# Kernel optimization log

Hardware: AMD Instinct MI355X
Metric: run time of the kernel (lower is better)

## Reference

```python
import jax, jax.numpy as jnp
import numpy as np

A, D, F = 2048, 64, 12  # atoms, depth, filter_length


def _chemconv(x, conn, bond, filters):
    # x: (A, D); conn: (A, A, F); bond: (A, F, 2); filters: (D, F, D+2)
    # node_connection = conn.transpose(1,2) @ x -> (A, F, D)
    ncon = jnp.einsum('anf,nd->afd', conn, x)
    combined = jnp.concatenate([ncon, bond], axis=2)  # (A, F, D+2)
    # broadcast-multiply by filters then sum over last two dims -> (A, out_depth)
    return jnp.einsum('afc,ofc->ao', combined, filters)


def setup_inputs() -> dict:
    key = jax.random.key(0)
    k1, k2, k3, k4, k5 = jax.random.split(key, 5)
    x = jax.random.normal(k1, (A, D), dtype=jnp.float32)
    conn = jax.random.uniform(k2, (A, A, F), dtype=jnp.float32)
    bond = jax.random.normal(k3, (A, F, 2), dtype=jnp.float32)
    scale = 1.0 / D  # filters.data.normal_() * (1/in_depth)
    f0 = jax.random.normal(k4, (D, F, D + 2), dtype=jnp.float32) * scale
    f1 = jax.random.normal(k5, (D, F, D + 2), dtype=jnp.float32) * scale
    return {
        'node_property_tensor': x,
        'connectivity_tensor': conn,
        'bond_property_tensor': bond,
        'filters0': f0,
        'filters1': f1,
    }


def reference(node_property_tensor, connectivity_tensor, bond_property_tensor, filters0, filters1):
    x = node_property_tensor
    out = x
    for filt in (filters0, filters1):
        # each ChemConv layer is applied twice (same weights), per the torch code
        out = jax.nn.relu(_chemconv(out, connectivity_tensor, bond_property_tensor, filt))
        out = _chemconv(out, connectivity_tensor, bond_property_tensor, filt)
        out = out + x  # residual to the original block input
        out = jax.nn.relu(out)
    return out
```

## Files before the change

### kernel.cpp

```cpp
#include <hip/hip_runtime.h>


#define A_N 2048
#define D_N 64
#define F_N 12
#define K_TOTAL (A_N * F_N)
#define NSPLIT 48
#define KSEG (K_TOTAL / NSPLIT)
#define BK 64
#define NKB (KSEG / BK)

typedef short short8 __attribute__((ext_vector_type(8)));
typedef float f32x16 __attribute__((ext_vector_type(16)));

#define GLOAD16(ldsp, gp)                                                        \
  __builtin_amdgcn_global_load_lds(                                              \
      (const __attribute__((address_space(1))) void*)(gp),                       \
      (__attribute__((address_space(3))) void*)(ldsp), 16, 0, 0)

__device__ __forceinline__ unsigned pk_bf16(float a, float b) {
  unsigned ua = __float_as_uint(a);
  unsigned ub = __float_as_uint(b);
  ua += 0x7fffu + ((ua >> 16) & 1u);
  ub += 0x7fffu + ((ub >> 16) & 1u);
  return (ua >> 16) | (ub & 0xffff0000u);
}

__global__ void k_conv(const float* __restrict__ conn, uint4* __restrict__ connb) {
  size_t i = (size_t)blockIdx.x * 256 + threadIdx.x;
  const float4* src = (const float4*)conn + i * 2;
  float4 c0 = src[0];
  float4 c1 = src[1];
  uint4 o;
  o.x = pk_bf16(c0.x, c0.y);
  o.y = pk_bf16(c0.z, c0.w);
  o.z = pk_bf16(c1.x, c1.y);
  o.w = pk_bf16(c1.z, c1.w);
  connb[i] = o;
}

__global__ void k_transpose_x(const float* __restrict__ x, float* __restrict__ xt) {
  __shared__ float ld[64][65];
  int m0 = blockIdx.x * 64;
  int t = threadIdx.x;
  int r = t >> 2, cq = (t & 3) * 16;
  const float4* src = (const float4*)(x + (size_t)(m0 + r) * 64 + cq);
#pragma unroll
  for (int i = 0; i < 4; ++i) {
    float4 v = src[i];
    ld[r][cq + i * 4 + 0] = v.x;
    ld[r][cq + i * 4 + 1] = v.y;
    ld[r][cq + i * 4 + 2] = v.z;
    ld[r][cq + i * 4 + 3] = v.w;
  }
  __syncthreads();
  int c = t >> 2, ml0 = (t & 3) * 16;
  float4* dst = (float4*)(xt + (size_t)c * 2048 + m0 + ml0);
#pragma unroll
  for (int i = 0; i < 4; ++i) {
    float4 v;
    v.x = ld[ml0 + i * 4 + 0][c];
    v.y = ld[ml0 + i * 4 + 1][c];
    v.z = ld[ml0 + i * 4 + 2][c];
    v.w = ld[ml0 + i * 4 + 3][c];
    dst[i] = v;
  }
}

__global__ void k_bterm(const float* __restrict__ bond, const float* __restrict__ f0,
                        const float* __restrict__ f1, float* __restrict__ bt0,
                        float* __restrict__ bt1) {
  int a = blockIdx.x * 64 + (threadIdx.x & 63);
  int o = blockIdx.y * 4 + (threadIdx.x >> 6);
  float s0 = 0.f, s1 = 0.f;
#pragma unroll
  for (int f = 0; f < F_N; ++f) {
#pragma unroll
    for (int j = 0; j < 2; ++j) {
      float bv = bond[a * 24 + f * 2 + j];
      s0 += bv * f0[o * 792 + f * 66 + 64 + j];
      s1 += bv * f1[o * 792 + f * 66 + 64 + j];
    }
  }
  bt0[o * 2048 + a] = s0;
  bt1[o * 2048 + a] = s1;
}

__global__ void k_g(const float* __restrict__ vt, const float* __restrict__ filt,
                    unsigned* __restrict__ gt ) {
  __shared__ float W[12][64];
  int o = blockIdx.y;
  int t = threadIdx.x;
  for (int i = t; i < 768; i += 256) W[i >> 6][i & 63] = filt[o * 792 + (i >> 6) * 66 + (i & 63)];
  __syncthreads();
  int n = blockIdx.x * 256 + t;
  float acc[12] = {0.f, 0.f, 0.f, 0.f, 0.f, 0.f, 0.f, 0.f, 0.f, 0.f, 0.f, 0.f};
#pragma unroll 4
  for (int d = 0; d < 64; ++d) {
    float v = vt[d * 2048 + n];
#pragma unroll
    for (int f = 0; f < F_N; ++f) acc[f] += v * W[f][d];
  }
  unsigned* dst = gt + ((size_t)o * K_TOTAL + n * 12) / 2;
#pragma unroll
  for (int i = 0; i < 6; ++i) dst[i] = pk_bf16(acc[2 * i], acc[2 * i + 1]);
}

__launch_bounds__(256, 3)
__global__ void k_big(const unsigned short* __restrict__ connb,
                      const unsigned short* __restrict__ gt, float* __restrict__ part) {
  __shared__ __align__(16) unsigned short smem[24576];
  int t = threadIdx.x, lane = t & 63, w = t >> 6;
  int m0 = blockIdx.x * 128;
  int k0 = blockIdx.y * KSEG;

  int rl = lane >> 3;
  int cs = (lane & 7) ^ rl;

  const unsigned short* cG[4];
  unsigned short* cL[4];
#pragma unroll
  for (int j = 0; j < 4; ++j) {
    int r = w * 32 + j * 8 + rl;
    cG[j] = connb + (size_t)(m0 + r) * K_TOTAL + k0 + cs * 8;
    cL[j] = smem + (w * 32 + j * 8) * 64;
  }
  const unsigned short* gG[2];
  unsigned short* gL[2];
#pragma unroll
  for (int j = 0; j < 2; ++j) {
    int r = w * 16 + j * 8 + rl;
    gG[j] = gt + (size_t)r * K_TOTAL + k0 + cs * 8;
    gL[j] = smem + 16384 + (w * 16 + j * 8) * 64;
  }

  f32x16 acc0, acc1;
#pragma unroll
  for (int i = 0; i < 16; ++i) { acc0[i] = 0.f; acc1[i] = 0.f; }

  int oh = w >> 1, ah = w & 1;
  int orow = oh * 32 + (lane & 31);
  int arow = ah * 64 + (lane & 31);
  int sw = lane & 7;
  int khalf = lane >> 5;

#pragma unroll
  for (int j = 0; j < 4; ++j) GLOAD16(cL[j], cG[j]);
#pragma unroll
  for (int j = 0; j < 2; ++j) GLOAD16(gL[j], gG[j]);

  for (int kb = 0; kb < NKB; ++kb) {
    __syncthreads();
    if (kb + 1 < NKB) {
      int ko = (kb + 1) * 64;
      int b = (kb + 1) & 1;
#pragma unroll
      for (int j = 0; j < 4; ++j) GLOAD16(cL[j] + b * 8192, cG[j] + ko);
#pragma unroll
      for (int j = 0; j < 2; ++j) GLOAD16(gL[j] + b * 4096, gG[j] + ko);
    }
    const unsigned short* cb = smem + (kb & 1) * 8192;
    const unsigned short* gb = smem + 16384 + (kb & 1) * 4096;
#pragma unroll
    for (int kk = 0; kk < 4; ++kk) {
      int c = kk * 2 + khalf;
      int coff = ((c ^ sw) << 3);
      short8 af = *(const short8*)(gb + orow * 64 + coff);
      short8 b0 = *(const short8*)(cb + arow * 64 + coff);
      short8 b1 = *(const short8*)(cb + (arow + 32) * 64 + coff);
      acc0 = __builtin_amdgcn_mfma_f32_32x32x16_bf16(af, b0, acc0, 0, 0, 0);
      acc1 = __builtin_amdgcn_mfma_f32_32x32x16_bf16(af, b1, acc1, 0, 0, 0);
    }
  }

  float* pp = part + (size_t)blockIdx.y * (64 * 2048);
  int a0 = m0 + ah * 64 + (lane & 31);
  int ob = oh * 32 + 4 * khalf;
#pragma unroll
  for (int rg = 0; rg < 16; ++rg) {
    int o = ob + (rg & 3) + 8 * (rg >> 2);
    pp[o * 2048 + a0] = acc0[rg];
    pp[o * 2048 + a0 + 32] = acc1[rg];
  }
}

__global__ void k_reduce(const float* __restrict__ part, const float* __restrict__ bt,
                         const float* __restrict__ xt, float* __restrict__ curt,
                         float* __restrict__ outp, int residual, int final_layer) {
  int idx = blockIdx.x * 256 + threadIdx.x;
  float s = bt[idx];
#pragma unroll
  for (int sI = 0; sI < NSPLIT; ++sI) s += part[(size_t)sI * (64 * 2048) + idx];
  if (residual) s += xt[idx];
  s = fmaxf(s, 0.f);
  curt[idx] = s;
  if (final_layer) {
    int o = idx >> 11, m = idx & 2047;
    outp[m * 64 + o] = s;
  }
}

extern "C" void kernel_launch(void* const* d_in, const int* in_sizes, int n_in,
                              void* d_out, int out_size, void* d_ws, size_t ws_size,
                              hipStream_t stream) {
  const float* x    = (const float*)d_in[0];
  const float* conn = (const float*)d_in[1];
  const float* bond = (const float*)d_in[2];
  const float* f0   = (const float*)d_in[3];
  const float* f1   = (const float*)d_in[4];
  float* out = (float*)d_out;

  char* ws = (char*)d_ws;
  float* xt   = (float*)(ws + 0);
  float* curt = (float*)(ws + 524288);
  float* bt0  = (float*)(ws + 1048576);
  float* bt1  = (float*)(ws + 1572864);
  unsigned short* gt = (unsigned short*)(ws + 2097152);
  float* part = (float*)(ws + 5242880);
  unsigned short* connb = (unsigned short*)(ws + 33554432);

  k_conv<<<24576, 256, 0, stream>>>(conn, (uint4*)connb);
  k_transpose_x<<<32, 256, 0, stream>>>(x, xt);
  k_bterm<<<dim3(32, 16), 256, 0, stream>>>(bond, f0, f1, bt0, bt1);

  for (int layer = 0; layer < 4; ++layer) {
    const float* filt = (layer < 2) ? f0 : f1;
    const float* bt   = (layer < 2) ? bt0 : bt1;
    const float* vin  = (layer == 0) ? xt : curt;
    k_g<<<dim3(8, 64), 256, 0, stream>>>(vin, filt, (unsigned*)gt);
    k_big<<<dim3(16, NSPLIT), 256, 0, stream>>>(connb, gt, part);
    k_reduce<<<512, 256, 0, stream>>>(part, bt, xt, curt, out, layer & 1, layer == 3);
  }
}
```

Before: 493.6 us.

## Pre-tile bf16 connectivity and g operands into contiguous per-block K-segment layout

```diff
diff --git a/kernel.cpp b/kernel.cpp
--- a/kernel.cpp
+++ b/kernel.cpp
@@ -26,17 +26,31 @@
   return (ua >> 16) | (ub & 0xffff0000u);
 }
 
-__global__ void k_conv(const float* __restrict__ conn, uint4* __restrict__ connb) {
-  size_t i = (size_t)blockIdx.x * 256 + threadIdx.x;
-  const float4* src = (const float4*)conn + i * 2;
-  float4 c0 = src[0];
-  float4 c1 = src[1];
-  uint4 o;
-  o.x = pk_bf16(c0.x, c0.y);
-  o.y = pk_bf16(c0.z, c0.w);
-  o.z = pk_bf16(c1.x, c1.y);
-  o.w = pk_bf16(c1.z, c1.w);
-  connb[i] = o;
+__device__ __forceinline__ unsigned short bf16_1(float v) {
+  unsigned u = __float_as_uint(v);
+  u += 0x7fffu + ((u >> 16) & 1u);
+  return (unsigned short)(u >> 16);
+}
+
+__global__ void k_conv(const float* __restrict__ conn, unsigned short* __restrict__ connt) {
+  int atile = blockIdx.x, ks = blockIdx.y;
+  int t = threadIdx.x, lane = t & 63, w = t >> 6;
+  unsigned short* tile = connt + (size_t)(atile * 48 + ks) * 65536;
+  int kb = lane >> 3, j = lane & 7;
+#pragma unroll 4
+  for (int p = 0; p < 32; ++p) {
+    int row = w * 32 + p;
+    const float4* src = (const float4*)(conn + (size_t)(atile * 128 + row) * K_TOTAL +
+                                        ks * 512 + lane * 8);
+    float4 a = src[0];
+    float4 b = src[1];
+    uint4 o;
+    o.x = pk_bf16(a.x, a.y);
+    o.y = pk_bf16(a.z, a.w);
+    o.z = pk_bf16(b.x, b.y);
+    o.w = pk_bf16(b.z, b.w);
+    *(uint4*)(tile + ((kb * 128 + row) * 8 + j) * 8) = o;
+  }
 }
 
 __global__ void k_transpose_x(const float* __restrict__ x, float* __restrict__ xt) {
@@ -87,7 +101,7 @@
 }
 
 __global__ void k_g(const float* __restrict__ vt, const float* __restrict__ filt,
-                    unsigned* __restrict__ gt ) {
+                    unsigned short* __restrict__ gtt) {
   __shared__ float W[12][64];
   int o = blockIdx.y;
   int t = threadIdx.x;
@@ -101,37 +115,38 @@
 #pragma unroll
     for (int f = 0; f < F_N; ++f) acc[f] += v * W[f][d];
   }
-  unsigned* dst = gt + ((size_t)o * K_TOTAL + n * 12) / 2;
-#pragma unroll
-  for (int i = 0; i < 6; ++i) dst[i] = pk_bf16(acc[2 * i], acc[2 * i + 1]);
+  int kbase = n * 12;
+#pragma unroll
+  for (int f = 0; f < F_N; ++f) {
+    int k = kbase + f;
+    int ks = k >> 9, kb = (k >> 6) & 7, c = k & 63;
+    gtt[(((size_t)ks * 8 + kb) * 64 + o) * 64 + c] = bf16_1(acc[f]);
+  }
 }
 
 __launch_bounds__(256, 3)
-__global__ void k_big(const unsigned short* __restrict__ connb,
-                      const unsigned short* __restrict__ gt, float* __restrict__ part) {
+__global__ void k_big(const unsigned short* __restrict__ connt,
+                      const unsigned short* __restrict__ gtt, float* __restrict__ part) {
   __shared__ __align__(16) unsigned short smem[24576];
   int t = threadIdx.x, lane = t & 63, w = t >> 6;
-  int m0 = blockIdx.x * 128;
-  int k0 = blockIdx.y * KSEG;
-
-  int rl = lane >> 3;
-  int cs = (lane & 7) ^ rl;
-
-  const unsigned short* cG[4];
-  unsigned short* cL[4];
+  int atile = blockIdx.x, ks = blockIdx.y;
+  const unsigned short* ct = connt + (size_t)(atile * 48 + ks) * 65536;
+  const unsigned short* gs = gtt + (size_t)ks * 32768;
+
+  int rl = lane >> 3, sl = lane & 7;
+  int cs = sl ^ rl;
+
+  int cSrc[4], gSrc[2];
+  unsigned short *cDst[4], *gDst[2];
 #pragma unroll
   for (int j = 0; j < 4; ++j) {
-    int r = w * 32 + j * 8 + rl;
-    cG[j] = connb + (size_t)(m0 + r) * K_TOTAL + k0 + cs * 8;
-    cL[j] = smem + (w * 32 + j * 8) * 64;
-  }
-  const unsigned short* gG[2];
-  unsigned short* gL[2];
+    cSrc[j] = (w * 32 + j * 8 + rl) * 64 + cs * 8;
+    cDst[j] = smem + (w * 32 + j * 8) * 64;
+  }
 #pragma unroll
   for (int j = 0; j < 2; ++j) {
-    int r = w * 16 + j * 8 + rl;
-    gG[j] = gt + (size_t)r * K_TOTAL + k0 + cs * 8;
-    gL[j] = smem + 16384 + (w * 16 + j * 8) * 64;
+    gSrc[j] = (w * 16 + j * 8 + rl) * 64 + cs * 8;
+    gDst[j] = smem + 16384 + (w * 16 + j * 8) * 64;
   }
 
   f32x16 acc0, acc1;
@@ -145,19 +160,19 @@
   int khalf = lane >> 5;
 
 #pragma unroll
-  for (int j = 0; j < 4; ++j) GLOAD16(cL[j], cG[j]);
-#pragma unroll
-  for (int j = 0; j < 2; ++j) GLOAD16(gL[j], gG[j]);
+  for (int j = 0; j < 4; ++j) GLOAD16(cDst[j], ct + cSrc[j]);
+#pragma unroll
+  for (int j = 0; j < 2; ++j) GLOAD16(gDst[j], gs + gSrc[j]);
 
   for (int kb = 0; kb < NKB; ++kb) {
     __syncthreads();
     if (kb + 1 < NKB) {
-      int ko = (kb + 1) * 64;
       int b = (kb + 1) & 1;
-#pragma unroll
-      for (int j = 0; j < 4; ++j) GLOAD16(cL[j] + b * 8192, cG[j] + ko);
-#pragma unroll
-      for (int j = 0; j < 2; ++j) GLOAD16(gL[j] + b * 4096, gG[j] + ko);
+      int co = (kb + 1) * 8192, go = (kb + 1) * 4096;
+#pragma unroll
+      for (int j = 0; j < 4; ++j) GLOAD16(cDst[j] + b * 8192, ct + co + cSrc[j]);
+#pragma unroll
+      for (int j = 0; j < 2; ++j) GLOAD16(gDst[j] + b * 4096, gs + go + gSrc[j]);
     }
     const unsigned short* cb = smem + (kb & 1) * 8192;
     const unsigned short* gb = smem + 16384 + (kb & 1) * 4096;
@@ -173,8 +188,8 @@
     }
   }
 
-  float* pp = part + (size_t)blockIdx.y * (64 * 2048);
-  int a0 = m0 + ah * 64 + (lane & 31);
+  float* pp = part + (size_t)ks * (64 * 2048);
+  int a0 = atile * 128 + ah * 64 + (lane & 31);
   int ob = oh * 32 + 4 * khalf;
 #pragma unroll
   for (int rg = 0; rg < 16; ++rg) {
@@ -215,11 +230,11 @@
   float* curt = (float*)(ws + 524288);
   float* bt0  = (float*)(ws + 1048576);
   float* bt1  = (float*)(ws + 1572864);
-  unsigned short* gt = (unsigned short*)(ws + 2097152);
+  unsigned short* gtt = (unsigned short*)(ws + 2097152);
   float* part = (float*)(ws + 5242880);
-  unsigned short* connb = (unsigned short*)(ws + 33554432);
-
-  k_conv<<<24576, 256, 0, stream>>>(conn, (uint4*)connb);
+  unsigned short* connt = (unsigned short*)(ws + 33554432);
+
+  k_conv<<<dim3(16, 48), 256, 0, stream>>>(conn, connt);
   k_transpose_x<<<32, 256, 0, stream>>>(x, xt);
   k_bterm<<<dim3(32, 16), 256, 0, stream>>>(bond, f0, f1, bt0, bt1);
 
@@ -227,8 +242,8 @@
     const float* filt = (layer < 2) ? f0 : f1;
     const float* bt   = (layer < 2) ? bt0 : bt1;
     const float* vin  = (layer == 0) ? xt : curt;
-    k_g<<<dim3(8, 64), 256, 0, stream>>>(vin, filt, (unsigned*)gt);
-    k_big<<<dim3(16, NSPLIT), 256, 0, stream>>>(connb, gt, part);
+    k_g<<<dim3(8, 64), 256, 0, stream>>>(vin, filt, gtt);
+    k_big<<<dim3(16, NSPLIT), 256, 0, stream>>>(connt, gtt, part);
     k_reduce<<<512, 256, 0, stream>>>(part, bt, xt, curt, out, layer & 1, layer == 3);
   }
 }
```

Measured after the change: 496.5 us. No clear change (+0.6%).
